# Kernel tuning notes

Measured on AMD Instinct MI355X. Metric: run time of the kernel, lower is better.

The kernel has to match this reference:

```python
import jax, jax.numpy as jnp
import numpy as np

K, B, T, D = 4, 4096, 32, 128


def setup_inputs() -> dict:
    key = jax.random.key(0)
    k1, k2, k3 = jax.random.split(key, 3)
    semb = jax.random.normal(k1, (K, B, D), dtype=jnp.float32)
    slabels = jax.random.randint(k2, (K, B), 0, 2, dtype=jnp.int32)
    topk_ngh = jax.random.randint(k3, (K, B, T), 0, B, dtype=jnp.int32)
    return {"semb": semb, "slabels": slabels, "topk_ngh": topk_ngh}


def reference(semb, slabels, topk_ngh):
    """Dense, masked reformulation of DistanceLayer.forward (hardest=False).

    Original emits, per domain k and anchor i, one triplet for every pair
    (sn, dn) where sn/dn are topk neighbors of i with same/different binary
    label, carrying sim[i,sn] (pos_dist), sim[i,dn] (neg_dist) and the anchor/
    pos/neg embeddings. Here we return the same quantities densified over the
    fixed [K,B,T,T] pair grid with a validity mask (jit-compatible shapes).
    Anchor embeddings are semb itself; pos/neg embeddings are rows of
    nbr_embed selected by the same/diff sides of pair_mask.
    """
    gather = jax.vmap(lambda tbl, idx: tbl[idx])  # per-domain row gather
    nbr_embed = gather(semb, topk_ngh)            # [K,B,T,D]
    nbr_label = gather(slabels, topk_ngh)         # [K,B,T]
    # sim[i, ngh[i,t]] without materializing the full [B,B] sim matrix
    nsim = jnp.einsum('kbd,kbtd->kbt', semb, nbr_embed)  # [K,B,T]
    same = nbr_label == slabels[:, :, None]       # neighbor shares anchor label
    pair_mask = same[:, :, :, None] & (~same)[:, :, None, :]  # [K,B,T,T]
    pos_dist = jnp.where(pair_mask, nsim[:, :, :, None], 0.0)  # sim(i, sn)
    neg_dist = jnp.where(pair_mask, nsim[:, :, None, :], 0.0)  # sim(i, dn)
    return pos_dist, neg_dist, pair_mask, nbr_embed
```

## Files before the change

### kernel.cpp

```cpp
#include <hip/hip_runtime.h>

constexpr int K = 4;
constexpr int B = 4096;
constexpr int T = 32;
constexpr int D = 128;
constexpr int TT = T * T;
constexpr int TD = T * D;

typedef float f4 __attribute__((ext_vector_type(4)));

__device__ __forceinline__ float dot4(f4 a, f4 b) {
    return a.x * b.x + a.y * b.y + a.z * b.z + a.w * b.w;
}

__device__ __forceinline__ float hreduce32(float p) {
    #pragma unroll
    for (int m = 16; m >= 1; m >>= 1) p += __shfl_xor(p, m, 64);
    return p;
}

struct __align__(16) WaveSh { float nsim[T]; };

__global__ __launch_bounds__(256) void distance_layer_kernel(
    const float* __restrict__ semb,
    const int*   __restrict__ slabels,
    const int*   __restrict__ topk,
    float* __restrict__ pos,
    float* __restrict__ neg,
    float* __restrict__ maskf,
    float* __restrict__ nbr)
{
    const int tid  = threadIdx.x;
    const int wid  = tid >> 6;
    const int l    = tid & 63;
    const int half = l >> 5;
    const int d4   = l & 31;

    const int kb = blockIdx.x * 4 + wid;
    const int k  = kb >> 12;

    __shared__ WaveSh sh[4];
    WaveSh& w = sh[wid];

    const int my_label = slabels[kb];
    const int idx_l    = topk[kb * T + d4];
    const int same_l   = (slabels[(k << 12) + idx_l] == my_label) ? 1 : 0;
    const unsigned mask = (unsigned)__ballot(same_l);

    const f4* semb4 = reinterpret_cast<const f4*>(semb + (size_t)k * B * D);
    f4*       nbr4  = reinterpret_cast<f4*>(nbr + (size_t)kb * TD);
    const f4  a     = reinterpret_cast<const f4*>(semb + (size_t)kb * D)[d4];

    #pragma unroll
    for (int g = 0; g < 2; ++g) {
        int ridx[8];
        #pragma unroll
        for (int j = 0; j < 8; ++j)
            ridx[j] = __shfl(idx_l, 16 * g + 2 * j + half, 64);

        f4 sv[8];
        #pragma unroll
        for (int j = 0; j < 8; ++j)
            sv[j] = semb4[(size_t)ridx[j] * (D / 4) + d4];

        #pragma unroll
        for (int j = 0; j < 8; ++j) {
            const int row = 16 * g + 2 * j + half;
            nbr4[row * (D / 4) + d4] = sv[j];
            const float p = hreduce32(dot4(a, sv[j]));
            if (d4 == 0) w.nsim[row] = p;
        }
    }

    const int d0 = (l & 7) * 4;
    const f4 ndv = *reinterpret_cast<const f4*>(&w.nsim[d0]);
    const unsigned md = (mask >> d0) & 0xFu;
    const int b0 =  md       & 1;
    const int b1 = (md >> 1) & 1;
    const int b2 = (md >> 2) & 1;
    const int b3 = (md >> 3) & 1;

    f4* pos4  = reinterpret_cast<f4*>(pos   + (size_t)kb * TT);
    f4* neg4  = reinterpret_cast<f4*>(neg   + (size_t)kb * TT);
    f4* mask4 = reinterpret_cast<f4*>(maskf + (size_t)kb * TT);

    #pragma unroll
    for (int i = 0; i < 4; ++i) {
        const int   s  = 8 * i + (l >> 3);
        const int   ss = (mask >> s) & 1;
        const float ps = w.nsim[s];

        const int m0 = ss & (b0 ^ 1);
        const int m1 = ss & (b1 ^ 1);
        const int m2 = ss & (b2 ^ 1);
        const int m3 = ss & (b3 ^ 1);

        f4 pv, nv, mv;
        pv.x = m0 ? ps : 0.0f;  nv.x = m0 ? ndv.x : 0.0f;  mv.x = (float)m0;
        pv.y = m1 ? ps : 0.0f;  nv.y = m1 ? ndv.y : 0.0f;  mv.y = (float)m1;
        pv.z = m2 ? ps : 0.0f;  nv.z = m2 ? ndv.z : 0.0f;  mv.z = (float)m2;
        pv.w = m3 ? ps : 0.0f;  nv.w = m3 ? ndv.w : 0.0f;  mv.w = (float)m3;

        pos4 [64 * i + l] = pv;
        neg4 [64 * i + l] = nv;
        mask4[64 * i + l] = mv;
    }
}

extern "C" void kernel_launch(void* const* d_in, const int* in_sizes, int n_in,
                              void* d_out, int out_size, void* d_ws, size_t ws_size,
                              hipStream_t stream) {
    const float* semb    = (const float*)d_in[0];
    const int*   slabels = (const int*)d_in[1];
    const int*   topk    = (const int*)d_in[2];

    float* out = (float*)d_out;
    const size_t KBTT = (size_t)K * B * T * T;
    float* pos   = out;
    float* neg   = out + KBTT;
    float* maskf = out + 2 * KBTT;
    float* nbr   = out + 3 * KBTT;

    distance_layer_kernel<<<dim3(K * B / 4), dim3(256), 0, stream>>>(
        semb, slabels, topk, pos, neg, maskf, nbr);
}
```

Baseline: 463.6 us.

## Split fused kernel into gather pass and per-output expand kernels

Splits the single fused kernel into a gather kernel that writes neighbor embeddings plus per-anchor similarities and label masks to workspace. Three templated expand kernels then each write one of the pos, neg and mask outputs. This aims to simplify each kernel's store stream and its register pressure on a write-bound workload. The cost is extra launches and a workspace round trip. The fused kernel remains as a fallback when the workspace is too small.

```diff
diff --git a/kernel.cpp b/kernel.cpp
--- a/kernel.cpp
+++ b/kernel.cpp
@@ -21,14 +21,14 @@
 
 struct __align__(16) WaveSh { float nsim[T]; };
 
-__global__ __launch_bounds__(256) void distance_layer_kernel(
+
+__global__ __launch_bounds__(256) void gather_kernel(
     const float* __restrict__ semb,
     const int*   __restrict__ slabels,
     const int*   __restrict__ topk,
-    float* __restrict__ pos,
-    float* __restrict__ neg,
-    float* __restrict__ maskf,
-    float* __restrict__ nbr)
+    float*       __restrict__ nbr,
+    float*       __restrict__ ws_nsim,
+    unsigned*    __restrict__ ws_mask)
 {
     const int tid  = threadIdx.x;
     const int wid  = tid >> 6;
@@ -72,13 +72,98 @@
         }
     }
 
+    if (l < 32) ws_nsim[kb * T + l] = w.nsim[l];
+    if (l == 0) ws_mask[kb] = mask;
+}
+
+template<int MODE>
+__global__ __launch_bounds__(256) void expand_kernel(
+    const float*    __restrict__ nsim,
+    const unsigned* __restrict__ maskw,
+    float*          __restrict__ out)
+{
+    const int tid = threadIdx.x;
+    const int s   = tid >> 3;
+    const int d0  = (tid & 7) * 4;
+    f4*       out4  = reinterpret_cast<f4*>(out);
+    const f4* nsim4 = reinterpret_cast<const f4*>(nsim);
+    const int base_kb = blockIdx.x * 8;
+
+    #pragma unroll
+    for (int j = 0; j < 8; ++j) {
+        const int kb = base_kb + j;
+        const unsigned m  = maskw[kb];
+        const int      ss = (m >> s) & 1;
+        const unsigned md = (m >> d0) & 0xFu;
+        const int m0 = ss & (((md >> 0) & 1) ^ 1);
+        const int m1 = ss & (((md >> 1) & 1) ^ 1);
+        const int m2 = ss & (((md >> 2) & 1) ^ 1);
+        const int m3 = ss & (((md >> 3) & 1) ^ 1);
+
+        f4 v;
+        if (MODE == 2) {
+            v.x = (float)m0; v.y = (float)m1; v.z = (float)m2; v.w = (float)m3;
+        } else if (MODE == 0) {
+            const float ps = nsim[kb * T + s];
+            v.x = m0 ? ps : 0.0f; v.y = m1 ? ps : 0.0f;
+            v.z = m2 ? ps : 0.0f; v.w = m3 ? ps : 0.0f;
+        } else {
+            const f4 nd = nsim4[kb * (T / 4) + (tid & 7)];
+            v.x = m0 ? nd.x : 0.0f; v.y = m1 ? nd.y : 0.0f;
+            v.z = m2 ? nd.z : 0.0f; v.w = m3 ? nd.w : 0.0f;
+        }
+        out4[(size_t)kb * (TT / 4) + tid] = v;
+    }
+}
+
+__global__ __launch_bounds__(256) void distance_layer_kernel(
+    const float* __restrict__ semb, const int* __restrict__ slabels,
+    const int* __restrict__ topk, float* __restrict__ pos,
+    float* __restrict__ neg, float* __restrict__ maskf, float* __restrict__ nbr)
+{
+    const int tid  = threadIdx.x;
+    const int wid  = tid >> 6;
+    const int l    = tid & 63;
+    const int half = l >> 5;
+    const int d4   = l & 31;
+    const int kb = blockIdx.x * 4 + wid;
+    const int k  = kb >> 12;
+
+    __shared__ WaveSh sh[4];
+    WaveSh& w = sh[wid];
+
+    const int my_label = slabels[kb];
+    const int idx_l    = topk[kb * T + d4];
+    const int same_l   = (slabels[(k << 12) + idx_l] == my_label) ? 1 : 0;
+    const unsigned mask = (unsigned)__ballot(same_l);
+
+    const f4* semb4 = reinterpret_cast<const f4*>(semb + (size_t)k * B * D);
+    f4*       nbr4  = reinterpret_cast<f4*>(nbr + (size_t)kb * TD);
+    const f4  a     = reinterpret_cast<const f4*>(semb + (size_t)kb * D)[d4];
+
+    #pragma unroll
+    for (int g = 0; g < 2; ++g) {
+        int ridx[8];
+        #pragma unroll
+        for (int j = 0; j < 8; ++j)
+            ridx[j] = __shfl(idx_l, 16 * g + 2 * j + half, 64);
+        f4 sv[8];
+        #pragma unroll
+        for (int j = 0; j < 8; ++j)
+            sv[j] = semb4[(size_t)ridx[j] * (D / 4) + d4];
+        #pragma unroll
+        for (int j = 0; j < 8; ++j) {
+            const int row = 16 * g + 2 * j + half;
+            nbr4[row * (D / 4) + d4] = sv[j];
+            const float p = hreduce32(dot4(a, sv[j]));
+            if (d4 == 0) w.nsim[row] = p;
+        }
+    }
+
     const int d0 = (l & 7) * 4;
     const f4 ndv = *reinterpret_cast<const f4*>(&w.nsim[d0]);
     const unsigned md = (mask >> d0) & 0xFu;
-    const int b0 =  md       & 1;
-    const int b1 = (md >> 1) & 1;
-    const int b2 = (md >> 2) & 1;
-    const int b3 = (md >> 3) & 1;
+    const int b0 = md & 1, b1 = (md >> 1) & 1, b2 = (md >> 2) & 1, b3 = (md >> 3) & 1;
 
     f4* pos4  = reinterpret_cast<f4*>(pos   + (size_t)kb * TT);
     f4* neg4  = reinterpret_cast<f4*>(neg   + (size_t)kb * TT);
@@ -89,18 +174,13 @@
         const int   s  = 8 * i + (l >> 3);
         const int   ss = (mask >> s) & 1;
         const float ps = w.nsim[s];
-
-        const int m0 = ss & (b0 ^ 1);
-        const int m1 = ss & (b1 ^ 1);
-        const int m2 = ss & (b2 ^ 1);
-        const int m3 = ss & (b3 ^ 1);
-
+        const int m0 = ss & (b0 ^ 1), m1 = ss & (b1 ^ 1);
+        const int m2 = ss & (b2 ^ 1), m3 = ss & (b3 ^ 1);
         f4 pv, nv, mv;
         pv.x = m0 ? ps : 0.0f;  nv.x = m0 ? ndv.x : 0.0f;  mv.x = (float)m0;
         pv.y = m1 ? ps : 0.0f;  nv.y = m1 ? ndv.y : 0.0f;  mv.y = (float)m1;
         pv.z = m2 ? ps : 0.0f;  nv.z = m2 ? ndv.z : 0.0f;  mv.z = (float)m2;
         pv.w = m3 ? ps : 0.0f;  nv.w = m3 ? ndv.w : 0.0f;  mv.w = (float)m3;
-
         pos4 [64 * i + l] = pv;
         neg4 [64 * i + l] = nv;
         mask4[64 * i + l] = mv;
@@ -121,6 +201,19 @@
     float* maskf = out + 2 * KBTT;
     float* nbr   = out + 3 * KBTT;
 
-    distance_layer_kernel<<<dim3(K * B / 4), dim3(256), 0, stream>>>(
-        semb, slabels, topk, pos, neg, maskf, nbr);
-}
+    const size_t NSIM_BYTES = (size_t)K * B * T * sizeof(float);
+    const size_t MASK_BYTES = (size_t)K * B * sizeof(unsigned);
+
+    if (ws_size >= NSIM_BYTES + MASK_BYTES) {
+        float*    ws_nsim = (float*)d_ws;
+        unsigned* ws_mask = (unsigned*)((char*)d_ws + NSIM_BYTES);
+        gather_kernel<<<dim3(K * B / 4), dim3(256), 0, stream>>>(
+            semb, slabels, topk, nbr, ws_nsim, ws_mask);
+        expand_kernel<0><<<dim3(K * B / 8), dim3(256), 0, stream>>>(ws_nsim, ws_mask, pos);
+        expand_kernel<1><<<dim3(K * B / 8), dim3(256), 0, stream>>>(ws_nsim, ws_mask, neg);
+        expand_kernel<2><<<dim3(K * B / 8), dim3(256), 0, stream>>>(ws_nsim, ws_mask, maskf);
+    } else {
+        distance_layer_kernel<<<dim3(K * B / 4), dim3(256), 0, stream>>>(
+            semb, slabels, topk, pos, neg, maskf, nbr);
+    }
+}
```

Result: no change. 472.3 us (+1.9%).
